# Kernel tuning notes

Measured on AMD Instinct MI355X. Metric: run time of the kernel, lower is better.

The kernel has to match this reference:

```python
import jax, jax.numpy as jnp
import numpy as np

K, N = 64, 4096

def setup_inputs() -> dict:
    key = jax.random.key(0)
    k1, k2 = jax.random.split(key)
    zs = jax.random.uniform(k1, (K, N), dtype=jnp.float32)        # K candidate schedules
    X = jax.random.uniform(k2, (N, N), dtype=jnp.float32)         # channel gain matrix
    var_noise = jnp.asarray(1.0, dtype=jnp.float32)
    return {"zs": zs, "X": X, "var_noise": var_noise}

def reference(zs, X, var_noise):
    # Original per-sample math: all_info[i,j] = z[j]*X[i,j]
    #   numerators   = diag(all_info) = z * diag(X)
    #   denominators = row_sum(all_info) - numerators = X @ z - numerators
    # Batched over K zs: one GEMM instead of K O(n^2) elementwise products.
    row_sums = jnp.einsum('kn,in->ki', zs, X)       # [K, N] = (X @ z_k)_i
    numerators = zs * jnp.diagonal(X)[None, :]      # [K, N]
    denominators = row_sums - numerators            # [K, N]
    per_sample = -jnp.sum(numerators / (var_noise + denominators), axis=1)  # [K]
    return jnp.sum(per_sample) / zs.shape[0]
```

## Files before the change

kernel.cpp:

```cpp
#include <hip/hip_runtime.h>

#define N_DIM 4096
#define NE    16

typedef float f4  __attribute__((ext_vector_type(4)));
typedef short s8v __attribute__((ext_vector_type(8)));

#if defined(__has_builtin)
#if __has_builtin(__builtin_amdgcn_cvt_pk_bf16_f32)
#define HAVE_CVT_PK 1
#endif
#endif

static __device__ __forceinline__ unsigned int f2bf_pair(float lo, float hi) {
#ifdef HAVE_CVT_PK
    typedef __bf16 bf2 __attribute__((ext_vector_type(2)));
    bf2 p = __builtin_amdgcn_cvt_pk_bf16_f32(lo, hi);
    return __builtin_bit_cast(unsigned int, p);
#else
    unsigned int ul = __builtin_bit_cast(unsigned int, lo);
    unsigned int uh = __builtin_bit_cast(unsigned int, hi);
    ul = ul + 0x7fffu + ((ul >> 16) & 1u);
    uh = uh + 0x7fffu + ((uh >> 16) & 1u);
    return (uh & 0xffff0000u) | (ul >> 16);
#endif
}

static __device__ __forceinline__ s8v cvt8(f4 a, f4 b) {
    unsigned int u4[4] = { f2bf_pair(a[0], a[1]), f2bf_pair(a[2], a[3]),
                           f2bf_pair(b[0], b[1]), f2bf_pair(b[2], b[3]) };
    return __builtin_bit_cast(s8v, u4);
}

#define MFMA(a, b, c) __builtin_amdgcn_mfma_f32_16x16x32_bf16((a), (b), (c), 0, 0, 0)

__global__ void zero_out_kernel(float* __restrict__ out) {
    if (threadIdx.x == 0 && blockIdx.x == 0) out[0] = 0.f;
}

__global__ __launch_bounds__(256) void gemm_part_kernel(
    const float* __restrict__ zs, const float* __restrict__ X,
    float* __restrict__ part) {
    __shared__ s8v zsP[2][512];
    __shared__ s8v xP [2][512];

    const int tid  = threadIdx.x;
    const int lane = tid & 63;
    const int w    = tid >> 6;
    const int n0   = blockIdx.x * 256;
    const int i0   = blockIdx.y * 64;

    const int r0  = tid >> 3;
    const int c8w = tid & 7;
    const int g0  = r0 * 8 + (c8w ^ (r0 & 7));
    const int g1  = g0 + 256;

    const float* gz0 = zs + (size_t)r0 * N_DIM + n0 + c8w * 8;
    const float* gz1 = gz0 + (size_t)32 * N_DIM;
    const float* gx0 = X  + (size_t)(i0 + r0) * N_DIM + n0 + c8w * 8;
    const float* gx1 = gx0 + (size_t)32 * N_DIM;

    f4 rz[4], rx[4];
    rz[0] = *(const f4*)(gz0);     rz[1] = *(const f4*)(gz0 + 4);
    rz[2] = *(const f4*)(gz1);     rz[3] = *(const f4*)(gz1 + 4);
    rx[0] = *(const f4*)(gx0);     rx[1] = *(const f4*)(gx0 + 4);
    rx[2] = *(const f4*)(gx1);     rx[3] = *(const f4*)(gx1 + 4);

    f4 acc[2][2] = {};
    const int kh = (w & 1) * 2;
    const int ih = (w >> 1) * 2;
    const int u0 = (lane & 15) * 8;
    const int xs0 = (lane >> 4) ^ (lane & 7);
    const int xs1 = xs0 ^ 4;

    for (int c = 0; c < 4; ++c) {
        const int buf = c & 1;
        s8v pz0 = cvt8(rz[0], rz[1]);
        s8v pz1 = cvt8(rz[2], rz[3]);
        s8v px0 = cvt8(rx[0], rx[1]);
        s8v px1 = cvt8(rx[2], rx[3]);
        if (c < 3) {
            const int off = (c + 1) * 64;
            rz[0] = *(const f4*)(gz0 + off); rz[1] = *(const f4*)(gz0 + off + 4);
            rz[2] = *(const f4*)(gz1 + off); rz[3] = *(const f4*)(gz1 + off + 4);
            rx[0] = *(const f4*)(gx0 + off); rx[1] = *(const f4*)(gx0 + off + 4);
            rx[2] = *(const f4*)(gx1 + off); rx[3] = *(const f4*)(gx1 + off + 4);
        }
        zsP[buf][g0] = pz0;  zsP[buf][g1] = pz1;
        xP[buf][g0]  = px0;  xP[buf][g1]  = px1;
        asm volatile("s_waitcnt lgkmcnt(0)\n\ts_barrier" ::: "memory");

        s8v a0s0 = zsP[buf][(kh    ) * 128 + u0 + xs0];
        s8v a0s1 = zsP[buf][(kh    ) * 128 + u0 + xs1];
        s8v a1s0 = zsP[buf][(kh + 1) * 128 + u0 + xs0];
        s8v a1s1 = zsP[buf][(kh + 1) * 128 + u0 + xs1];
        s8v b0s0 = xP [buf][(ih    ) * 128 + u0 + xs0];
        s8v b0s1 = xP [buf][(ih    ) * 128 + u0 + xs1];
        s8v b1s0 = xP [buf][(ih + 1) * 128 + u0 + xs0];
        s8v b1s1 = xP [buf][(ih + 1) * 128 + u0 + xs1];

        acc[0][0] = MFMA(a0s0, b0s0, acc[0][0]);
        acc[0][1] = MFMA(a0s0, b1s0, acc[0][1]);
        acc[1][0] = MFMA(a1s0, b0s0, acc[1][0]);
        acc[1][1] = MFMA(a1s0, b1s0, acc[1][1]);
        acc[0][0] = MFMA(a0s1, b0s1, acc[0][0]);
        acc[0][1] = MFMA(a0s1, b1s1, acc[0][1]);
        acc[1][0] = MFMA(a1s1, b0s1, acc[1][0]);
        acc[1][1] = MFMA(a1s1, b1s1, acc[1][1]);
    }

    f4* pp = (f4*)part;
    const int tb = (blockIdx.y * NE + blockIdx.x) * 1024;
    #pragma unroll
    for (int a = 0; a < 2; ++a)
        #pragma unroll
        for (int b = 0; b < 2; ++b)
            pp[tb + ((kh + a) * 4 + (ih + b)) * 64 + lane] = acc[a][b];
}

__global__ __launch_bounds__(256) void epilogue_kernel(
    const float* __restrict__ part, const float* __restrict__ zs,
    const float* __restrict__ X, const float* __restrict__ varp,
    float* __restrict__ out) {
    const int tid  = threadIdx.x;
    const int lane = tid & 63;
    const int w    = tid >> 6;
    const int ib   = blockIdx.x;
    const f4* pp   = (const f4*)part;

    f4 s[4] = {};
    for (int ne = 0; ne < NE; ++ne) {
        const f4* q = pp + (ib * NE + ne) * 1024 + tid * 4;
        #pragma unroll
        for (int jj = 0; jj < 4; ++jj) s[jj] += q[jj];
    }
    const int j0  = tid * 4;
    const int kt  = j0 >> 8;
    const int itl = (j0 >> 6) & 3;
    const int ln0 = j0 & 63;
    const int k0  = kt * 16 + (ln0 >> 4) * 4;
    const int ibs = ib * 64 + itl * 16 + (ln0 & 15);
    const float var = varp[0];

    float vsum = 0.f;
    #pragma unroll
    for (int c2 = 0; c2 < 4; ++c2) {
        const int   i  = ibs + c2;
        const float dg = X[(size_t)i * (N_DIM + 1)];
        #pragma unroll
        for (int r = 0; r < 4; ++r) {
            float num = zs[(size_t)(k0 + r) * N_DIM + i] * dg;
            float den = s[c2][r] - num;
            vsum += num / (var + den);
        }
    }
    #pragma unroll
    for (int off = 32; off >= 1; off >>= 1) vsum += __shfl_down(vsum, off);
    __shared__ float wsum[4];
    if (lane == 0) wsum[w] = vsum;
    __syncthreads();
    if (tid == 0)
        atomicAdd(out, -(wsum[0] + wsum[1] + wsum[2] + wsum[3]) * (1.0f / 64.0f));
}

extern "C" void kernel_launch(void* const* d_in, const int* in_sizes, int n_in,
                              void* d_out, int out_size, void* d_ws, size_t ws_size,
                              hipStream_t stream) {
    const float* zs   = (const float*)d_in[0];
    const float* X    = (const float*)d_in[1];
    const float* varp = (const float*)d_in[2];
    float* out  = (float*)d_out;
    float* part = (float*)d_ws;

    hipLaunchKernelGGL(zero_out_kernel, dim3(1), dim3(64), 0, stream, out);
    hipLaunchKernelGGL(gemm_part_kernel, dim3(NE, 64), dim3(256), 0, stream, zs, X, part);
    hipLaunchKernelGGL(epilogue_kernel, dim3(64), dim3(256), 0, stream,
                       part, zs, X, varp, out);
}
```

Measured before the change: 109.8 us.

## Double-buffer global prefetch in GEMM, widen epilogue grid, use memset for zeroing

The GEMM kernel now prefetches two K-chunks ahead into register double buffers with a fully unrolled loop, so more global loads are in flight while MFMA work runs. The epilogue is split across a 4x64 grid, with each thread reducing one f4 of partials instead of four, which raises parallelism for the reduction over the partial buffer. The zeroing kernel is replaced with hipMemsetAsync. The extra prefetch buffers cost more registers, and the larger epilogue grid performs four times as many atomics.

```diff
diff --git a/kernel.cpp b/kernel.cpp
--- a/kernel.cpp
+++ b/kernel.cpp
@@ -34,10 +34,6 @@
 
 #define MFMA(a, b, c) __builtin_amdgcn_mfma_f32_16x16x32_bf16((a), (b), (c), 0, 0, 0)
 
-__global__ void zero_out_kernel(float* __restrict__ out) {
-    if (threadIdx.x == 0 && blockIdx.x == 0) out[0] = 0.f;
-}
-
 __global__ __launch_bounds__(256) void gemm_part_kernel(
     const float* __restrict__ zs, const float* __restrict__ X,
     float* __restrict__ part) {
@@ -60,31 +56,36 @@
     const float* gx0 = X  + (size_t)(i0 + r0) * N_DIM + n0 + c8w * 8;
     const float* gx1 = gx0 + (size_t)32 * N_DIM;
 
-    f4 rz[4], rx[4];
-    rz[0] = *(const f4*)(gz0);     rz[1] = *(const f4*)(gz0 + 4);
-    rz[2] = *(const f4*)(gz1);     rz[3] = *(const f4*)(gz1 + 4);
-    rx[0] = *(const f4*)(gx0);     rx[1] = *(const f4*)(gx0 + 4);
-    rx[2] = *(const f4*)(gx1);     rx[3] = *(const f4*)(gx1 + 4);
+    f4 rz[2][4], rx[2][4];
+    #pragma unroll
+    for (int p = 0; p < 2; ++p) {
+        const int off = p * 64;
+        rz[p][0] = *(const f4*)(gz0 + off); rz[p][1] = *(const f4*)(gz0 + off + 4);
+        rz[p][2] = *(const f4*)(gz1 + off); rz[p][3] = *(const f4*)(gz1 + off + 4);
+        rx[p][0] = *(const f4*)(gx0 + off); rx[p][1] = *(const f4*)(gx0 + off + 4);
+        rx[p][2] = *(const f4*)(gx1 + off); rx[p][3] = *(const f4*)(gx1 + off + 4);
+    }
 
     f4 acc[2][2] = {};
-    const int kh = (w & 1) * 2;
-    const int ih = (w >> 1) * 2;
-    const int u0 = (lane & 15) * 8;
+    const int kh  = (w & 1) * 2;
+    const int ih  = (w >> 1) * 2;
+    const int u0  = (lane & 15) * 8;
     const int xs0 = (lane >> 4) ^ (lane & 7);
     const int xs1 = xs0 ^ 4;
 
+    #pragma unroll
     for (int c = 0; c < 4; ++c) {
         const int buf = c & 1;
-        s8v pz0 = cvt8(rz[0], rz[1]);
-        s8v pz1 = cvt8(rz[2], rz[3]);
-        s8v px0 = cvt8(rx[0], rx[1]);
-        s8v px1 = cvt8(rx[2], rx[3]);
-        if (c < 3) {
-            const int off = (c + 1) * 64;
-            rz[0] = *(const f4*)(gz0 + off); rz[1] = *(const f4*)(gz0 + off + 4);
-            rz[2] = *(const f4*)(gz1 + off); rz[3] = *(const f4*)(gz1 + off + 4);
-            rx[0] = *(const f4*)(gx0 + off); rx[1] = *(const f4*)(gx0 + off + 4);
-            rx[2] = *(const f4*)(gx1 + off); rx[3] = *(const f4*)(gx1 + off + 4);
+        s8v pz0 = cvt8(rz[buf][0], rz[buf][1]);
+        s8v pz1 = cvt8(rz[buf][2], rz[buf][3]);
+        s8v px0 = cvt8(rx[buf][0], rx[buf][1]);
+        s8v px1 = cvt8(rx[buf][2], rx[buf][3]);
+        if (c < 2) {
+            const int off = (c + 2) * 64;
+            rz[buf][0] = *(const f4*)(gz0 + off); rz[buf][1] = *(const f4*)(gz0 + off + 4);
+            rz[buf][2] = *(const f4*)(gz1 + off); rz[buf][3] = *(const f4*)(gz1 + off + 4);
+            rx[buf][0] = *(const f4*)(gx0 + off); rx[buf][1] = *(const f4*)(gx0 + off + 4);
+            rx[buf][2] = *(const f4*)(gx1 + off); rx[buf][3] = *(const f4*)(gx1 + off + 4);
         }
         zsP[buf][g0] = pz0;  zsP[buf][g1] = pz1;
         xP[buf][g0]  = px0;  xP[buf][g1]  = px1;
@@ -125,34 +126,28 @@
     const int tid  = threadIdx.x;
     const int lane = tid & 63;
     const int w    = tid >> 6;
-    const int ib   = blockIdx.x;
+    const int q    = blockIdx.x;
+    const int it   = blockIdx.y;
     const f4* pp   = (const f4*)part;
 
-    f4 s[4] = {};
+    f4 s = {};
+    const int jj = q * 256 + tid;
+    #pragma unroll 4
     for (int ne = 0; ne < NE; ++ne) {
-        const f4* q = pp + (ib * NE + ne) * 1024 + tid * 4;
-        #pragma unroll
-        for (int jj = 0; jj < 4; ++jj) s[jj] += q[jj];
+        f4 v = pp[(it * NE + ne) * 1024 + jj];
+        s[0] += v[0]; s[1] += v[1]; s[2] += v[2]; s[3] += v[3];
     }
-    const int j0  = tid * 4;
-    const int kt  = j0 >> 8;
-    const int itl = (j0 >> 6) & 3;
-    const int ln0 = j0 & 63;
-    const int k0  = kt * 16 + (ln0 >> 4) * 4;
-    const int ibs = ib * 64 + itl * 16 + (ln0 & 15);
+    const int   i   = it * 64 + w * 16 + (lane & 15);
+    const int   k0  = q * 16 + (lane >> 4) * 4;
+    const float dg  = X[(size_t)i * (N_DIM + 1)];
     const float var = varp[0];
 
     float vsum = 0.f;
     #pragma unroll
-    for (int c2 = 0; c2 < 4; ++c2) {
-        const int   i  = ibs + c2;
-        const float dg = X[(size_t)i * (N_DIM + 1)];
-        #pragma unroll
-        for (int r = 0; r < 4; ++r) {
-            float num = zs[(size_t)(k0 + r) * N_DIM + i] * dg;
-            float den = s[c2][r] - num;
-            vsum += num / (var + den);
-        }
+    for (int r = 0; r < 4; ++r) {
+        float num = zs[(size_t)(k0 + r) * N_DIM + i] * dg;
+        float den = s[r] - num;
+        vsum += num / (var + den);
     }
     #pragma unroll
     for (int off = 32; off >= 1; off >>= 1) vsum += __shfl_down(vsum, off);
@@ -172,8 +167,8 @@
     float* out  = (float*)d_out;
     float* part = (float*)d_ws;
 
-    hipLaunchKernelGGL(zero_out_kernel, dim3(1), dim3(64), 0, stream, out);
+    hipMemsetAsync(out, 0, sizeof(float), stream);
     hipLaunchKernelGGL(gemm_part_kernel, dim3(NE, 64), dim3(256), 0, stream, zs, X, part);
-    hipLaunchKernelGGL(epilogue_kernel, dim3(64), dim3(256), 0, stream,
+    hipLaunchKernelGGL(epilogue_kernel, dim3(4, 64), dim3(256), 0, stream,
                        part, zs, X, varp, out);
 }
```

Result: no change. 110.0 us (+0.2%).
